# Performance work log

Measured on AMD Instinct MI355X. Metric: run time of the kernel, lower is better.

## Reference

```python
import jax, jax.numpy as jnp
import numpy as np

B, N, M, K, QK, GEO = 2, 16384, 4096, 16, 64, 18
EPS = 1e-5


def _conv1d(x, w, b):  # x [B,C,N], w [O,C] -> [B,O,N]  (1x1 Conv1d)
    return jnp.einsum('oc,bcn->bon', w, x) + b[None, :, None]


def _bn1d(x, g, bt):  # train-mode BatchNorm1d: batch stats over (B, N)
    m = x.mean(axis=(0, 2), keepdims=True)
    v = x.var(axis=(0, 2), keepdims=True)
    return (x - m) * jax.lax.rsqrt(v + EPS) * g[None, :, None] + bt[None, :, None]


def _conv2d(x, w, b):  # x [B,C,N,K], w [O,C] -> [B,O,N,K]  (1x1 Conv2d)
    return jnp.einsum('oc,bcnk->bonk', w, x) + b[None, :, None, None]


def _bn2d(x, g, bt):
    m = x.mean(axis=(0, 2, 3), keepdims=True)
    v = x.var(axis=(0, 2, 3), keepdims=True)
    return (x - m) * jax.lax.rsqrt(v + EPS) * g[None, :, None, None] + bt[None, :, None, None]


def _gather(t, idx):  # t [B,C,M], idx [B,N,K] -> [B,C,N,K]; t_g[b,c,n,j] = t[b,c,idx[b,n,j]]
    return jnp.take_along_axis(t[:, :, None, :], idx[:, None, :, :], axis=3)


def setup_inputs() -> dict:
    key = jax.random.key(0)
    ks = iter(jax.random.split(key, 40))
    def rn(shape, s=0.02):
        return jax.random.normal(next(ks), shape, jnp.float32) * s
    def z(c):
        return jnp.zeros((c,), jnp.float32)
    def o(c):
        return jnp.ones((c,), jnp.float32)
    return dict(
        xyz_hr=jax.random.normal(next(ks), (B, 3, N), jnp.float32),
        xyz_lr=jax.random.normal(next(ks), (B, 3, M), jnp.float32),
        val_lr=jax.random.normal(next(ks), (B, 6, M), jnp.float32),
        feat_hr=jax.random.normal(next(ks), (B, GEO, N), jnp.float32),
        feat_lr=jax.random.normal(next(ks), (B, GEO, M), jnp.float32),
        ge_w1=rn((QK, GEO)), ge_b1=z(QK), ge_g1=o(QK), ge_bt1=z(QK),
        ge_w2=rn((QK, QK)), ge_b2=z(QK), ge_g2=o(QK), ge_bt2=z(QK),
        sc_w=rn((QK, 6)), sc_b=z(QK), sh_w=rn((QK, 6)), sh_b=z(QK),
        q_w=rn((QK, QK)), q_b=z(QK), k_w=rn((QK, QK)), k_b=z(QK),
        bh_w1=rn((32, QK)), bh_b1=z(32), bh_g=o(32), bh_bt=z(32),
        bh_w2=rn((1, 32)), bh_b2=z(1),
        rp_w1=rn((QK, 3)), rp_b1=z(QK), rp_g=o(QK), rp_bt=z(QK),
        rp_w2=rn((QK, QK)), rp_b2=z(QK),
    )


def reference(xyz_hr, xyz_lr, val_lr, feat_hr, feat_lr,
              ge_w1, ge_b1, ge_g1, ge_bt1, ge_w2, ge_b2, ge_g2, ge_bt2,
              sc_w, sc_b, sh_w, sh_b, q_w, q_b, k_w, k_b,
              bh_w1, bh_b1, bh_g, bh_bt, bh_w2, bh_b2,
              rp_w1, rp_b1, rp_g, rp_bt, rp_w2, rp_b2):
    def geom_enc(x):
        x = jax.nn.relu(_bn1d(_conv1d(x, ge_w1, ge_b1), ge_g1, ge_bt1))
        return jax.nn.relu(_bn1d(_conv1d(x, ge_w2, ge_b2), ge_g2, ge_bt2))

    geom_hr = geom_enc(feat_hr)   # [B,QK,N]
    geom_lr = geom_enc(feat_lr)   # [B,QK,M]

    # val_lr has 6 channels -> FiLM modulation branch is taken
    scale = _conv1d(val_lr, sc_w, sc_b)
    shift = _conv1d(val_lr, sh_w, sh_b)
    geom_lr = geom_lr * (scale + 1.0) + shift

    bdy = jax.nn.relu(_bn1d(_conv1d(geom_hr, bh_w1, bh_b1), bh_g, bh_bt))
    bdy_prob = jax.nn.sigmoid(_conv1d(bdy, bh_w2, bh_b2))  # [B,1,N]

    Q = _conv1d(geom_hr, q_w, q_b)   # [B,QK,N]
    Kf = _conv1d(geom_lr, k_w, k_b)  # [B,QK,M]

    # kNN under no_grad: squared euclidean via expansion (same ordering as cdist)
    a = xyz_hr.transpose(0, 2, 1)  # [B,N,3]
    b = xyz_lr.transpose(0, 2, 1)  # [B,M,3]
    d2 = (jnp.sum(a * a, -1)[:, :, None] + jnp.sum(b * b, -1)[:, None, :]
          - 2.0 * jnp.einsum('bnc,bmc->bnm', a, b))
    d2 = jax.lax.stop_gradient(d2)
    _, idx = jax.lax.top_k(-d2, K)  # [B,N,K] indices of K nearest low-res points

    K_g = _gather(Kf, idx)            # [B,QK,N,K]
    xyz_lr_g = _gather(xyz_lr, idx)   # [B,3,N,K]
    rel_pos = xyz_hr[:, :, :, None] - xyz_lr_g
    pe = jax.nn.relu(_bn2d(_conv2d(rel_pos, rp_w1, rp_b1), rp_g, rp_bt))
    pos_enc = _conv2d(pe, rp_w2, rp_b2)  # [B,QK,N,K]

    scores = jnp.einsum('bcn,bcnk->bnk', Q, K_g + pos_enc) / jnp.sqrt(jnp.float32(QK))
    attn = jax.nn.softmax(scores, axis=-1)          # [B,N,K]
    val_g = _gather(val_lr, idx)                    # [B,6,N,K]
    out = jnp.einsum('bnk,bcnk->bcn', attn, val_g)  # [B,6,N]
    return out, bdy_prob
```

## Files before the change

kernel.cpp:

```cpp
#include <hip/hip_runtime.h>

#define BB 2
#define NN 16384
#define MM 4096
#define KK 16
#define CQ 64
#define GEOC 18
#define EPSV 1e-5
#define SPL 8

__device__ __forceinline__ float dist2f(float sa, float ax, float ay, float az, float4 p) {
#pragma clang fp contract(off)
  return (sa + p.w) - 2.0f * ((ax * p.x + ay * p.y) + az * p.z);
}

__device__ __forceinline__ void ce(float& a, float& b) {
  float lo = fminf(a, b), hi = fmaxf(a, b); a = lo; b = hi;
}
__device__ __forceinline__ void sort8(float* v) {
  ce(v[0],v[1]); ce(v[2],v[3]); ce(v[4],v[5]); ce(v[6],v[7]);
  ce(v[0],v[2]); ce(v[1],v[3]); ce(v[4],v[6]); ce(v[5],v[7]);
  ce(v[1],v[2]); ce(v[5],v[6]);
  ce(v[0],v[4]); ce(v[1],v[5]); ce(v[2],v[6]); ce(v[3],v[7]);
  ce(v[2],v[4]); ce(v[3],v[5]);
  ce(v[1],v[2]); ce(v[3],v[4]); ce(v[5],v[6]);
}
__device__ __forceinline__ void bitonic16(float* v) {
#pragma unroll
  for (int i = 0; i < 8; i++) ce(v[i], v[i + 8]);
  ce(v[0],v[4]); ce(v[1],v[5]); ce(v[2],v[6]); ce(v[3],v[7]);
  ce(v[8],v[12]); ce(v[9],v[13]); ce(v[10],v[14]); ce(v[11],v[15]);
  ce(v[0],v[2]); ce(v[1],v[3]); ce(v[4],v[6]); ce(v[5],v[7]);
  ce(v[8],v[10]); ce(v[9],v[11]); ce(v[12],v[14]); ce(v[13],v[15]);
  ce(v[0],v[1]); ce(v[2],v[3]); ce(v[4],v[5]); ce(v[6],v[7]);
  ce(v[8],v[9]); ce(v[10],v[11]); ce(v[12],v[13]); ce(v[14],v[15]);
}
__device__ __forceinline__ void merge16_8(float* dv, const float* t) {
  dv[8]  = fminf(dv[8],  t[7]);  dv[9]  = fminf(dv[9],  t[6]);
  dv[10] = fminf(dv[10], t[5]);  dv[11] = fminf(dv[11], t[4]);
  dv[12] = fminf(dv[12], t[3]);  dv[13] = fminf(dv[13], t[2]);
  dv[14] = fminf(dv[14], t[1]);  dv[15] = fminf(dv[15], t[0]);
  bitonic16(dv);
}

__global__ __launch_bounds__(256) void init_k(const float* __restrict__ xyz,
    const float* __restrict__ val, float* __restrict__ xyzT, float* __restrict__ valT,
    const float* __restrict__ qw, const float* __restrict__ qb, const float* __restrict__ w2,
    float* __restrict__ R, float* __restrict__ rb, int* __restrict__ hdr)
{
#pragma clang fp contract(off)
  if (blockIdx.x < 32) {
    int i = blockIdx.x * 256 + threadIdx.x;
    int b = i / MM, m = i % MM;
    float x = xyz[(b * 3 + 0) * MM + m];
    float y = xyz[(b * 3 + 1) * MM + m];
    float z = xyz[(b * 3 + 2) * MM + m];
    float sb = (x * x + y * y) + z * z;
    ((float4*)xyzT)[i] = make_float4(x, y, z, sb);
    float v0 = val[((size_t)b * 6 + 0) * MM + m];
    float v1 = val[((size_t)b * 6 + 1) * MM + m];
    float v2 = val[((size_t)b * 6 + 2) * MM + m];
    float v3 = val[((size_t)b * 6 + 3) * MM + m];
    float v4 = val[((size_t)b * 6 + 4) * MM + m];
    float v5 = val[((size_t)b * 6 + 5) * MM + m];
    ((float4*)valT)[2 * i]     = make_float4(v0, v1, v2, v3);
    ((float4*)valT)[2 * i + 1] = make_float4(v4, v5, 0.f, 0.f);
  } else {
    int t = threadIdx.x;
    for (int wd = t; wd < 1376; wd += 256) hdr[wd] = 0;
#pragma unroll
    for (int e = t * 16; e < t * 16 + 16; e++) {
      int o = e >> 6, i = e & 63;
      float acc = 0.f;
#pragma unroll
      for (int p = 0; p < CQ; p++) acc = fmaf(w2[p * CQ + o], qw[p * CQ + i], acc);
      R[e] = acc;
    }
    if (t < CQ) {
      float a = 0.f;
#pragma unroll
      for (int p = 0; p < CQ; p++) a = fmaf(w2[p * CQ + t], qb[p], a);
      rb[t] = a;
    }
  }
}

template<int CIN, int COUT, int OBLK, bool TOUT>
__device__ __forceinline__ void conv_body(int tid, const float* __restrict__ x,
    const float* __restrict__ W, const float* __restrict__ bias,
    const float* __restrict__ AB, float* __restrict__ y, int L)
{
  int g = tid / (BB * L);
  int i = tid % (BB * L);
  int b = i / L, n = i % L;
  const float* xp = x + (size_t)b * CIN * L + n;
  float xr[CIN];
#pragma unroll
  for (int c = 0; c < CIN; c++) {
    float v = xp[(size_t)c * L];
    if (AB) v = fmaxf(fmaf(v, AB[c], AB[CIN + c]), 0.f);
    xr[c] = v;
  }
#pragma unroll
  for (int oo = 0; oo < OBLK; oo++) {
    int o = g * OBLK + oo;
    float acc = bias ? bias[o] : 0.f;
#pragma unroll
    for (int c = 0; c < CIN; c++)
      acc = fmaf(W[(size_t)o * CIN + c], xr[c], acc);
    if (TOUT) y[((size_t)b * L + n) * COUT + o] = acc;
    else      y[((size_t)b * COUT + o) * L + n] = acc;
  }
}

template<int CIN, int COUT, int OBLK>
__global__ __launch_bounds__(256) void convhl_k(const float* __restrict__ xh,
    const float* __restrict__ xl, const float* __restrict__ W, const float* __restrict__ bias,
    const float* __restrict__ ABh, const float* __restrict__ ABl,
    float* __restrict__ yh, float* __restrict__ yl, int hb)
{
  if ((int)blockIdx.x < hb)
    conv_body<CIN, COUT, OBLK, false>(blockIdx.x * 256 + threadIdx.x, xh, W, bias, ABh, yh, NN);
  else
    conv_body<CIN, COUT, OBLK, false>((blockIdx.x - hb) * 256 + threadIdx.x, xl, W, bias, ABl, yl, MM);
}

template<int C, int NCH>
__device__ __forceinline__ void stats_body(int bid, const float* __restrict__ t, int L,
    const float* __restrict__ g, const float* __restrict__ bt,
    double* __restrict__ sums, int* __restrict__ counter, float* __restrict__ AB)
{
  int c = bid % C;
  int ch = bid / C;
  const size_t tot = (size_t)BB * L;
  const size_t slab = tot / NCH;
  size_t beg = slab * ch, end = beg + slab;
  double s = 0.0, ss = 0.0;
  for (size_t idx = beg + threadIdx.x; idx < end; idx += 256) {
    int b = (int)(idx / L); int i = (int)(idx % L);
    double v = t[((size_t)b * C + c) * L + i];
    s += v; ss += v * v;
  }
  for (int o = 32; o >= 1; o >>= 1) { s += __shfl_down(s, o); ss += __shfl_down(ss, o); }
  __shared__ double sh[8];
  __shared__ int lastf;
  int w = threadIdx.x >> 6;
  if ((threadIdx.x & 63) == 0) { sh[2 * w] = s; sh[2 * w + 1] = ss; }
  __syncthreads();
  if (threadIdx.x == 0) {
    for (int j = 1; j < 4; j++) { s += sh[2 * j]; ss += sh[2 * j + 1]; }
    atomicAdd(&sums[c], s);
    atomicAdd(&sums[C + c], ss);
    __threadfence();
    int old = atomicAdd(counter, 1);
    lastf = (old == C * NCH - 1) ? 1 : 0;
  }
  __syncthreads();
  if (lastf && threadIdx.x < C) {
    __threadfence();
    int cc = threadIdx.x;
    double S  = atomicAdd(&sums[cc], 0.0);
    double SS = atomicAdd(&sums[C + cc], 0.0);
    double nn = (double)BB * L;
    double mean = S / nn, var = SS / nn - mean * mean;
    double A = (double)g[cc] / sqrt(var + EPSV);
    AB[cc] = (float)A;
    AB[C + cc] = (float)((double)bt[cc] - mean * A);
  }
}

template<int C, int NCH>
__global__ __launch_bounds__(256) void statsone_k(const float* __restrict__ t, int L,
    const float* __restrict__ g, const float* __restrict__ bt,
    double* __restrict__ sums, int* __restrict__ counter, float* __restrict__ AB)
{
  stats_body<C, NCH>(blockIdx.x, t, L, g, bt, sums, counter, AB);
}

template<int C, int NCH>
__global__ __launch_bounds__(256) void statshl_k(const float* __restrict__ t0, int L0,
    const float* __restrict__ t1, int L1, const float* __restrict__ g,
    const float* __restrict__ bt, double* __restrict__ sums, int* __restrict__ ctrs,
    float* __restrict__ AB0, float* __restrict__ AB1)
{
  if ((int)blockIdx.x < C * NCH)
    stats_body<C, NCH>(blockIdx.x, t0, L0, g, bt, sums, ctrs, AB0);
  else
    stats_body<C, NCH>(blockIdx.x - C * NCH, t1, L1, g, bt, sums + 2 * C, ctrs + 1, AB1);
}

__global__ __launch_bounds__(256) void fk_k(const float* __restrict__ t2l,
    const float* __restrict__ ABl, const float* __restrict__ val,
    const float* __restrict__ scw, const float* __restrict__ scb,
    const float* __restrict__ shw, const float* __restrict__ shb,
    const float* __restrict__ kw, const float* __restrict__ kb,
    float* __restrict__ KfT)
{
  int tid = blockIdx.x * 256 + threadIdx.x;
  int g = tid & 7;
  int i = tid >> 3;
  int b = i / MM, m = i % MM;
  float v6[6];
#pragma unroll
  for (int j = 0; j < 6; j++) v6[j] = val[((size_t)b * 6 + j) * MM + m];
  float xr[CQ];
#pragma unroll
  for (int c = 0; c < CQ; c++) {
    float gv = fmaxf(fmaf(t2l[((size_t)b * CQ + c) * MM + m], ABl[c], ABl[CQ + c]), 0.f);
    float sc = scb[c], sh = shb[c];
#pragma unroll
    for (int j = 0; j < 6; j++) {
      sc = fmaf(scw[c * 6 + j], v6[j], sc);
      sh = fmaf(shw[c * 6 + j], v6[j], sh);
    }
    xr[c] = fmaf(gv, 1.f + sc, sh);
  }
#pragma unroll
  for (int oo = 0; oo < 8; oo++) {
    int o = g * 8 + oo;
    float acc = kb[o];
#pragma unroll
    for (int c = 0; c < CQ; c++) acc = fmaf(kw[o * CQ + c], xr[c], acc);
    KfT[(size_t)i * CQ + o] = acc;
  }
}

__global__ __launch_bounds__(256) void convbqq_k(const float* __restrict__ x,
    const float* __restrict__ bw, const float* __restrict__ bb,
    const float* __restrict__ Wq, const float* __restrict__ bq,
    const float* __restrict__ R, const float* __restrict__ rb,
    const float* __restrict__ AB, float* __restrict__ tb,
    float* __restrict__ Q, float* __restrict__ Qp)
{
  int tid = blockIdx.x * 256 + threadIdx.x;
  int g = tid / (BB * NN);
  int i = tid % (BB * NN);
  int b = i / NN, n = i % NN;
  const float* xp = x + (size_t)b * CQ * NN + n;
  float xr[CQ];
#pragma unroll
  for (int c = 0; c < CQ; c++)
    xr[c] = fmaxf(fmaf(xp[(size_t)c * NN], AB[c], AB[CQ + c]), 0.f);
  const float* W; const float* bias; float* y; int o0;
  if (g < 2)      { W = bw; bias = bb; y = tb; o0 = g * 16;       }
  else if (g < 6) { W = Wq; bias = bq; y = Q;  o0 = (g - 2) * 16; }
  else            { W = R;  bias = rb; y = Qp; o0 = (g - 6) * 16; }
  int COUTL = (g < 2) ? 32 : CQ;
#pragma unroll
  for (int oo = 0; oo < 16; oo++) {
    int o = o0 + oo;
    float acc = bias[o];
#pragma unroll
    for (int c = 0; c < CQ; c++) acc = fmaf(W[o * CQ + c], xr[c], acc);
    y[((size_t)b * COUTL + o) * NN + n] = acc;
  }
}

__global__ __launch_bounds__(256) void knnA_k(const float* __restrict__ xyz_hr,
    const float* __restrict__ xyzT, float* __restrict__ theta)
{
#pragma clang fp contract(off)
  int tid = blockIdx.x * 256 + threadIdx.x;
  int s = tid & (SPL - 1);
  int qi = tid / SPL;
  int b = qi / NN, n = qi % NN;
  float ax = xyz_hr[(b * 3 + 0) * NN + n];
  float ay = xyz_hr[(b * 3 + 1) * NN + n];
  float az = xyz_hr[(b * 3 + 2) * NN + n];
  float sa = (ax * ax + ay * ay) + az * az;
  const float4* __restrict__ Ps = ((const float4*)xyzT) + (size_t)b * MM + s;
  float dv[16];
#pragma unroll
  for (int j = 0; j < 16; j++) dv[j] = 3.4e38f;
  for (int j = 0; j < MM / SPL; j += 8) {
    float t[8];
#pragma unroll
    for (int u = 0; u < 8; u++) {
      float4 p = Ps[(size_t)(j + u) * SPL];
      t[u] = dist2f(sa, ax, ay, az, p);
    }
    sort8(t);
    merge16_8(dv, t);
  }
#pragma unroll
  for (int mask = 1; mask <= 4; mask <<= 1) {
    float c[16];
#pragma unroll
    for (int j = 0; j < 16; j++) c[j] = __shfl_xor(dv[15 - j], mask);
#pragma unroll
    for (int j = 0; j < 16; j++) dv[j] = fminf(dv[j], c[j]);
    bitonic16(dv);
  }
  if (s == 0) theta[qi] = dv[15];
}

__global__ __launch_bounds__(256) void knnC_k(const float* __restrict__ xyz_hr,
    const float* __restrict__ xyzT, const float* __restrict__ theta,
    int* __restrict__ idx_out, double* __restrict__ mompart)
{
#pragma clang fp contract(off)
  __shared__ int s_clt[32], s_ceq[32];
  __shared__ int s_lt[32][16];
  __shared__ int s_eq[32][64];
  __shared__ int s_sel[32][16];
  __shared__ float s_mom[4][9];
  int w = threadIdx.x >> 6, l = threadIdx.x & 63;
  int qblk = blockIdx.x * 32;
  int b = qblk / NN;
  int n0 = qblk % NN + w * 8;
  if (threadIdx.x < 32) { s_clt[threadIdx.x] = 0; s_ceq[threadIdx.x] = 0; }
  __syncthreads();
  float qx[8], qy[8], qz[8], qs[8], th[8];
#pragma unroll
  for (int q = 0; q < 8; q++) {
    qx[q] = xyz_hr[(b * 3 + 0) * NN + n0 + q];
    qy[q] = xyz_hr[(b * 3 + 1) * NN + n0 + q];
    qz[q] = xyz_hr[(b * 3 + 2) * NN + n0 + q];
    qs[q] = (qx[q] * qx[q] + qy[q] * qy[q]) + qz[q] * qz[q];
    th[q] = theta[(size_t)b * NN + n0 + q];
  }
  const float4* __restrict__ P = ((const float4*)xyzT) + (size_t)b * MM;
  for (int j = 0; j < MM / 64; j++) {
    int m = j * 64 + l;
    float4 p = P[m];
#pragma unroll
    for (int q = 0; q < 8; q++) {
      float d = (qs[q] + p.w) - 2.0f * ((qx[q] * p.x + qy[q] * p.y) + qz[q] * p.z);
      int qq = w * 8 + q;
      if (d < th[q]) {
        int pos = atomicAdd(&s_clt[qq], 1);
        if (pos < 16) s_lt[qq][pos] = m;
      } else if (d == th[q]) {
        int pos = atomicAdd(&s_ceq[qq], 1);
        if (pos < 64) s_eq[qq][pos] = m;
      }
    }
  }
  __syncthreads();
  if (threadIdx.x < 32) {
    int qq = threadIdx.x;
    int clt = s_clt[qq]; if (clt > 16) clt = 16;
    int ceq = s_ceq[qq]; if (ceq > 64) ceq = 64;
    for (int j = 0; j < clt; j++) s_sel[qq][j] = s_lt[qq][j];
    int need = KK - clt;
    for (int t = 0; t < need; t++) {
      int best = 0x7fffffff, bp = 0;
      for (int j = 0; j < ceq; j++) { int v = s_eq[qq][j]; if (v < best) { best = v; bp = j; } }
      s_sel[qq][clt + t] = best;
      s_eq[qq][bp] = 0x7fffffff;
    }
    size_t base = ((size_t)qblk + qq) * KK;
    for (int j = 0; j < KK; j++) idx_out[base + j] = s_sel[qq][j];
  }
  __syncthreads();
  float t9[9];
#pragma unroll
  for (int j = 0; j < 9; j++) t9[j] = 0.f;
  for (int slot = threadIdx.x; slot < 512; slot += 256) {
    int qq = slot >> 4, jj = slot & 15;
    int nn_ = qblk % NN + qq;
    float ax = xyz_hr[(b * 3 + 0) * NN + nn_];
    float ay = xyz_hr[(b * 3 + 1) * NN + nn_];
    float az = xyz_hr[(b * 3 + 2) * NN + nn_];
    float4 p = P[s_sel[qq][jj]];
    float rx = ax - p.x, ry = ay - p.y, rz = az - p.z;
    t9[0] += rx; t9[1] += ry; t9[2] += rz;
    t9[3] += rx * rx; t9[4] += ry * ry; t9[5] += rz * rz;
    t9[6] += rx * ry; t9[7] += rx * rz; t9[8] += ry * rz;
  }
#pragma unroll
  for (int j = 0; j < 9; j++)
    for (int o = 32; o >= 1; o >>= 1) t9[j] += __shfl_down(t9[j], o);
  if (l == 0) { for (int j = 0; j < 9; j++) s_mom[w][j] = t9[j]; }
  __syncthreads();
  if (threadIdx.x == 0) {
    double* op = mompart + (size_t)blockIdx.x * 9;
    for (int j = 0; j < 9; j++)
      op[j] = (double)s_mom[0][j] + (double)s_mom[1][j] + (double)s_mom[2][j] + (double)s_mom[3][j];
  }
}

__global__ __launch_bounds__(256) void mom2_k(const double* __restrict__ part, int nblk,
    const float* __restrict__ w1, const float* __restrict__ b1,
    const float* __restrict__ g, const float* __restrict__ bt, float* __restrict__ AB)
{
  double acc[9];
#pragma unroll
  for (int j = 0; j < 9; j++) acc[j] = 0.0;
  for (int blk = threadIdx.x; blk < nblk; blk += 256) {
    const double* p = part + (size_t)blk * 9;
#pragma unroll
    for (int j = 0; j < 9; j++) acc[j] += p[j];
  }
#pragma unroll
  for (int j = 0; j < 9; j++)
    for (int o = 32; o >= 1; o >>= 1) acc[j] += __shfl_down(acc[j], o);
  __shared__ double sh[4][9];
  __shared__ double mo[9];
  int w = threadIdx.x >> 6, l = threadIdx.x & 63;
  if (l == 0) { for (int j = 0; j < 9; j++) sh[w][j] = acc[j]; }
  __syncthreads();
  if (threadIdx.x == 0) {
    for (int wv = 1; wv < 4; wv++) for (int j = 0; j < 9; j++) sh[0][j] += sh[wv][j];
    for (int j = 0; j < 9; j++) mo[j] = sh[0][j];
  }
  __syncthreads();
  if (threadIdx.x < CQ) {
    int c = threadIdx.x;
    double cnt = (double)BB * NN * KK;
    double mx = mo[0]/cnt, my = mo[1]/cnt, mz = mo[2]/cnt;
    double cxx = mo[3]/cnt - mx*mx, cyy = mo[4]/cnt - my*my, czz = mo[5]/cnt - mz*mz;
    double cxy = mo[6]/cnt - mx*my, cxz = mo[7]/cnt - mx*mz, cyz = mo[8]/cnt - my*mz;
    double wx = w1[c*3], wy = w1[c*3+1], wz = w1[c*3+2];
    double mean = wx*mx + wy*my + wz*mz + (double)b1[c];
    double var = wx*wx*cxx + wy*wy*cyy + wz*wz*czz + 2.0*(wx*wy*cxy + wx*wz*cxz + wy*wz*cyz);
    double A = (double)g[c] / sqrt(var + EPSV);
    AB[c] = (float)A;
    AB[CQ + c] = (float)((double)bt[c] - mean * A);
  }
}

__global__ __launch_bounds__(256) void attn_k(
    const float* __restrict__ Q, const float* __restrict__ Qp,
    const float* __restrict__ KfT, const int* __restrict__ idxb,
    const float* __restrict__ xyzT, const float* __restrict__ valT,
    const float* __restrict__ xyz_hr, const float* __restrict__ AB,
    const float* __restrict__ w1, const float* __restrict__ b1,
    const float* __restrict__ b2, float* __restrict__ out,
    const float* __restrict__ tb, const float* __restrict__ ABb,
    const float* __restrict__ bhw2, const float* __restrict__ bhb2)
{
  __shared__ float q_s[CQ * 16], qp_s[CQ * 16];
  if (blockIdx.x >= 2048) {
    int i = (blockIdx.x - 2048) * 256 + threadIdx.x;
    int b = i / NN, n = i % NN;
    float acc = bhb2[0];
#pragma unroll
    for (int c = 0; c < 32; c++) {
      float v = tb[((size_t)b * 32 + c) * NN + n];
      v = fmaxf(fmaf(v, ABb[c], ABb[32 + c]), 0.f);
      acc = fmaf(bhw2[c], v, acc);
    }
    out[(size_t)BB * 6 * NN + i] = 1.f / (1.f + expf(-acc));
    return;
  }
  const int ngrp = NN / 16;
  int b = blockIdx.x / ngrp;
  int n0 = (blockIdx.x % ngrp) * 16;
  for (int t = threadIdx.x; t < CQ * 16; t += 256) {
    int c = t >> 4, j = t & 15;
    q_s[t]  = Q [((size_t)b * CQ + c) * NN + n0 + j];
    qp_s[t] = Qp[((size_t)b * CQ + c) * NN + n0 + j];
  }
  __syncthreads();
  int q = threadIdx.x >> 4, k = threadIdx.x & 15;
  int n = n0 + q;
  int id = idxb[((size_t)b * NN + n) * KK + k];
  float ax = xyz_hr[(b * 3 + 0) * NN + n];
  float ay = xyz_hr[(b * 3 + 1) * NN + n];
  float az = xyz_hr[(b * 3 + 2) * NN + n];
  float4 pl = ((const float4*)xyzT)[(size_t)b * MM + id];
  float rx = ax - pl.x, ry = ay - pl.y, rz = az - pl.z;
  const float4* kg = (const float4*)(KfT + ((size_t)b * MM + id) * CQ);
  float s = 0.f;
#pragma unroll
  for (int c4 = 0; c4 < CQ / 4; c4++) {
    float4 g4 = kg[c4];
    float ga[4] = {g4.x, g4.y, g4.z, g4.w};
#pragma unroll
    for (int u = 0; u < 4; u++) {
      int c = 4 * c4 + u;
      float t0 = fmaf(w1[c * 3 + 0], rx, fmaf(w1[c * 3 + 1], ry, w1[c * 3 + 2] * rz)) + b1[c];
      float pe = fmaxf(fmaf(t0, AB[c], AB[CQ + c]), 0.f);
      s = fmaf(q_s[c * 16 + q], ga[u] + b2[c], s);
      s = fmaf(qp_s[c * 16 + q], pe, s);
    }
  }
  s *= 0.125f;
  float mx = s;
#pragma unroll
  for (int o = 8; o >= 1; o >>= 1) mx = fmaxf(mx, __shfl_xor(mx, o, 16));
  float p = expf(s - mx);
  float sum = p;
#pragma unroll
  for (int o = 8; o >= 1; o >>= 1) sum += __shfl_xor(sum, o, 16);
  float attn = p / sum;
  const float4* vt = (const float4*)(valT + ((size_t)b * MM + id) * 8);
  float4 va = vt[0], vb = vt[1];
  float oc[6] = {attn*va.x, attn*va.y, attn*va.z, attn*va.w, attn*vb.x, attn*vb.y};
#pragma unroll
  for (int c = 0; c < 6; c++) {
    float a = oc[c];
#pragma unroll
    for (int o = 8; o >= 1; o >>= 1) a += __shfl_xor(a, o, 16);
    oc[c] = a;
  }
  if (k == 0) {
#pragma unroll
    for (int c = 0; c < 6; c++) out[((size_t)b * 6 + c) * NN + n] = oc[c];
  }
}

extern "C" void kernel_launch(void* const* d_in, const int* in_sizes, int n_in,
                              void* d_out, int out_size, void* d_ws, size_t ws_size,
                              hipStream_t stream)
{
  const float* xyz_hr = (const float*)d_in[0];
  const float* xyz_lr = (const float*)d_in[1];
  const float* val_lr = (const float*)d_in[2];
  const float* feat_hr= (const float*)d_in[3];
  const float* feat_lr= (const float*)d_in[4];
  const float* ge_w1 = (const float*)d_in[5];
  const float* ge_b1 = (const float*)d_in[6];
  const float* ge_g1 = (const float*)d_in[7];
  const float* ge_bt1= (const float*)d_in[8];
  const float* ge_w2 = (const float*)d_in[9];
  const float* ge_b2 = (const float*)d_in[10];
  const float* ge_g2 = (const float*)d_in[11];
  const float* ge_bt2= (const float*)d_in[12];
  const float* sc_w = (const float*)d_in[13];
  const float* sc_b = (const float*)d_in[14];
  const float* sh_w = (const float*)d_in[15];
  const float* sh_b = (const float*)d_in[16];
  const float* q_w  = (const float*)d_in[17];
  const float* q_b  = (const float*)d_in[18];
  const float* k_w  = (const float*)d_in[19];
  const float* k_b  = (const float*)d_in[20];
  const float* bh_w1= (const float*)d_in[21];
  const float* bh_b1= (const float*)d_in[22];
  const float* bh_g = (const float*)d_in[23];
  const float* bh_bt= (const float*)d_in[24];
  const float* bh_w2= (const float*)d_in[25];
  const float* bh_b2= (const float*)d_in[26];
  const float* rp_w1= (const float*)d_in[27];
  const float* rp_b1= (const float*)d_in[28];
  const float* rp_g = (const float*)d_in[29];
  const float* rp_bt= (const float*)d_in[30];
  const float* rp_w2= (const float*)d_in[31];
  const float* rp_b2= (const float*)d_in[32];
  float* out = (float*)d_out;

  int*    hdr  = (int*)d_ws;
  int*    ctrs = (int*)((char*)d_ws + 96);
  double* sums = (double*)((char*)d_ws + 128);
  float*  base = (float*)((char*)d_ws + 5504);
  float* AB1h = base;
  float* AB2h = base + 128;
  float* AB1l = base + 256;
  float* AB2l = base + 384;
  float* ABb  = base + 512;
  float* AB2d = base + 576;
  float* big  = base + 768;
  float* t1_hr = big;
  float* t2_hr = t1_hr + 2097152;
  float* Qb    = t2_hr + 2097152;
  float* Qp    = Qb    + 2097152;
  float* t1_lr = Qp    + 2097152;
  float* t2_lr = t1_lr + 524288;
  float* Rbuf  = t2_lr + 524288;
  float* KfT   = Rbuf  + 524288;
  float* tb    = KfT   + 524288;
  float* xyzT  = tb    + 1048576;
  float* valT  = xyzT  + 32768;
  int*   idxb  = (int*)(valT + 65536);
  float* theta = Qb;
  double* mompart = (double*)Qp;
  float* Rw    = Rbuf;
  float* rbv   = Rbuf + 4096;

  init_k<<<33, 256, 0, stream>>>(xyz_lr, val_lr, xyzT, valT, q_w, q_b, rp_w2, Rw, rbv, hdr);

  knnA_k<<<(BB * NN * SPL) / 256, 256, 0, stream>>>(xyz_hr, xyzT, theta);
  knnC_k<<<(BB * NN) / 32, 256, 0, stream>>>(xyz_hr, xyzT, theta, idxb, mompart);
  mom2_k<<<1, 256, 0, stream>>>(mompart, (BB * NN) / 32, rp_w1, rp_b1, rp_g, rp_bt, AB2d);

  convhl_k<GEOC, CQ, 16><<<640, 256, 0, stream>>>(feat_hr, feat_lr, ge_w1, ge_b1,
                                                  nullptr, nullptr, t1_hr, t1_lr, 512);
  statshl_k<CQ, 8><<<1024, 256, 0, stream>>>(t1_hr, NN, t1_lr, MM, ge_g1, ge_bt1,
                                             sums, ctrs + 0, AB1h, AB1l);
  convhl_k<CQ, CQ, 16><<<640, 256, 0, stream>>>(t1_hr, t1_lr, ge_w2, ge_b2,
                                                AB1h, AB1l, t2_hr, t2_lr, 512);
  statshl_k<CQ, 8><<<1024, 256, 0, stream>>>(t2_hr, NN, t2_lr, MM, ge_g2, ge_bt2,
                                             sums + 256, ctrs + 2, AB2h, AB2l);

  fk_k<<<256, 256, 0, stream>>>(t2_lr, AB2l, val_lr, sc_w, sc_b, sh_w, sh_b,
                                k_w, k_b, KfT);

  convbqq_k<<<1280, 256, 0, stream>>>(t2_hr, bh_w1, bh_b1, q_w, q_b, Rw, rbv,
                                      AB2h, tb, Qb, Qp);
  statsone_k<32, 8><<<256, 256, 0, stream>>>(tb, NN, bh_g, bh_bt, sums + 512, ctrs + 4, ABb);

  attn_k<<<2048 + 128, 256, 0, stream>>>(Qb, Qp, KfT, idxb, xyzT, valT, xyz_hr, AB2d,
                                         rp_w1, rp_b1, rp_b2, out, tb, ABb, bh_w2, bh_b2);
}
```

Measured before the change: 530.9 us.

## Fuse kNN, conv and BatchNorm stats kernels into fewer combined launches

Merges the separate 1x1 conv and BatchNorm-statistics kernels by computing per-channel sums in shared memory right after each conv block, using a last-block-done counter to finalize the scale and shift. The independent kNN passes are co-scheduled in the same launches as the conv layers, and mom2, fk and convbqq are grouped into one kernel. This cuts the launch count from about ten to four and removes the re-reads of the conv outputs for statistics. In exchange it adds shared-memory reductions and atomics, gives heterogeneous blocks in each grid, and moves mompart to its own buffer.

New measurement: 463.4 us. 1.15x faster.

```diff
diff --git a/kernel.cpp b/kernel.cpp
--- a/kernel.cpp
+++ b/kernel.cpp
@@ -85,182 +85,10 @@
   }
 }
 
-template<int CIN, int COUT, int OBLK, bool TOUT>
-__device__ __forceinline__ void conv_body(int tid, const float* __restrict__ x,
-    const float* __restrict__ W, const float* __restrict__ bias,
-    const float* __restrict__ AB, float* __restrict__ y, int L)
-{
-  int g = tid / (BB * L);
-  int i = tid % (BB * L);
-  int b = i / L, n = i % L;
-  const float* xp = x + (size_t)b * CIN * L + n;
-  float xr[CIN];
-#pragma unroll
-  for (int c = 0; c < CIN; c++) {
-    float v = xp[(size_t)c * L];
-    if (AB) v = fmaxf(fmaf(v, AB[c], AB[CIN + c]), 0.f);
-    xr[c] = v;
-  }
-#pragma unroll
-  for (int oo = 0; oo < OBLK; oo++) {
-    int o = g * OBLK + oo;
-    float acc = bias ? bias[o] : 0.f;
-#pragma unroll
-    for (int c = 0; c < CIN; c++)
-      acc = fmaf(W[(size_t)o * CIN + c], xr[c], acc);
-    if (TOUT) y[((size_t)b * L + n) * COUT + o] = acc;
-    else      y[((size_t)b * COUT + o) * L + n] = acc;
-  }
-}
-
-template<int CIN, int COUT, int OBLK>
-__global__ __launch_bounds__(256) void convhl_k(const float* __restrict__ xh,
-    const float* __restrict__ xl, const float* __restrict__ W, const float* __restrict__ bias,
-    const float* __restrict__ ABh, const float* __restrict__ ABl,
-    float* __restrict__ yh, float* __restrict__ yl, int hb)
-{
-  if ((int)blockIdx.x < hb)
-    conv_body<CIN, COUT, OBLK, false>(blockIdx.x * 256 + threadIdx.x, xh, W, bias, ABh, yh, NN);
-  else
-    conv_body<CIN, COUT, OBLK, false>((blockIdx.x - hb) * 256 + threadIdx.x, xl, W, bias, ABl, yl, MM);
-}
-
-template<int C, int NCH>
-__device__ __forceinline__ void stats_body(int bid, const float* __restrict__ t, int L,
-    const float* __restrict__ g, const float* __restrict__ bt,
-    double* __restrict__ sums, int* __restrict__ counter, float* __restrict__ AB)
-{
-  int c = bid % C;
-  int ch = bid / C;
-  const size_t tot = (size_t)BB * L;
-  const size_t slab = tot / NCH;
-  size_t beg = slab * ch, end = beg + slab;
-  double s = 0.0, ss = 0.0;
-  for (size_t idx = beg + threadIdx.x; idx < end; idx += 256) {
-    int b = (int)(idx / L); int i = (int)(idx % L);
-    double v = t[((size_t)b * C + c) * L + i];
-    s += v; ss += v * v;
-  }
-  for (int o = 32; o >= 1; o >>= 1) { s += __shfl_down(s, o); ss += __shfl_down(ss, o); }
-  __shared__ double sh[8];
-  __shared__ int lastf;
-  int w = threadIdx.x >> 6;
-  if ((threadIdx.x & 63) == 0) { sh[2 * w] = s; sh[2 * w + 1] = ss; }
-  __syncthreads();
-  if (threadIdx.x == 0) {
-    for (int j = 1; j < 4; j++) { s += sh[2 * j]; ss += sh[2 * j + 1]; }
-    atomicAdd(&sums[c], s);
-    atomicAdd(&sums[C + c], ss);
-    __threadfence();
-    int old = atomicAdd(counter, 1);
-    lastf = (old == C * NCH - 1) ? 1 : 0;
-  }
-  __syncthreads();
-  if (lastf && threadIdx.x < C) {
-    __threadfence();
-    int cc = threadIdx.x;
-    double S  = atomicAdd(&sums[cc], 0.0);
-    double SS = atomicAdd(&sums[C + cc], 0.0);
-    double nn = (double)BB * L;
-    double mean = S / nn, var = SS / nn - mean * mean;
-    double A = (double)g[cc] / sqrt(var + EPSV);
-    AB[cc] = (float)A;
-    AB[C + cc] = (float)((double)bt[cc] - mean * A);
-  }
-}
-
-template<int C, int NCH>
-__global__ __launch_bounds__(256) void statsone_k(const float* __restrict__ t, int L,
-    const float* __restrict__ g, const float* __restrict__ bt,
-    double* __restrict__ sums, int* __restrict__ counter, float* __restrict__ AB)
-{
-  stats_body<C, NCH>(blockIdx.x, t, L, g, bt, sums, counter, AB);
-}
-
-template<int C, int NCH>
-__global__ __launch_bounds__(256) void statshl_k(const float* __restrict__ t0, int L0,
-    const float* __restrict__ t1, int L1, const float* __restrict__ g,
-    const float* __restrict__ bt, double* __restrict__ sums, int* __restrict__ ctrs,
-    float* __restrict__ AB0, float* __restrict__ AB1)
-{
-  if ((int)blockIdx.x < C * NCH)
-    stats_body<C, NCH>(blockIdx.x, t0, L0, g, bt, sums, ctrs, AB0);
-  else
-    stats_body<C, NCH>(blockIdx.x - C * NCH, t1, L1, g, bt, sums + 2 * C, ctrs + 1, AB1);
-}
-
-__global__ __launch_bounds__(256) void fk_k(const float* __restrict__ t2l,
-    const float* __restrict__ ABl, const float* __restrict__ val,
-    const float* __restrict__ scw, const float* __restrict__ scb,
-    const float* __restrict__ shw, const float* __restrict__ shb,
-    const float* __restrict__ kw, const float* __restrict__ kb,
-    float* __restrict__ KfT)
-{
-  int tid = blockIdx.x * 256 + threadIdx.x;
-  int g = tid & 7;
-  int i = tid >> 3;
-  int b = i / MM, m = i % MM;
-  float v6[6];
-#pragma unroll
-  for (int j = 0; j < 6; j++) v6[j] = val[((size_t)b * 6 + j) * MM + m];
-  float xr[CQ];
-#pragma unroll
-  for (int c = 0; c < CQ; c++) {
-    float gv = fmaxf(fmaf(t2l[((size_t)b * CQ + c) * MM + m], ABl[c], ABl[CQ + c]), 0.f);
-    float sc = scb[c], sh = shb[c];
-#pragma unroll
-    for (int j = 0; j < 6; j++) {
-      sc = fmaf(scw[c * 6 + j], v6[j], sc);
-      sh = fmaf(shw[c * 6 + j], v6[j], sh);
-    }
-    xr[c] = fmaf(gv, 1.f + sc, sh);
-  }
-#pragma unroll
-  for (int oo = 0; oo < 8; oo++) {
-    int o = g * 8 + oo;
-    float acc = kb[o];
-#pragma unroll
-    for (int c = 0; c < CQ; c++) acc = fmaf(kw[o * CQ + c], xr[c], acc);
-    KfT[(size_t)i * CQ + o] = acc;
-  }
-}
-
-__global__ __launch_bounds__(256) void convbqq_k(const float* __restrict__ x,
-    const float* __restrict__ bw, const float* __restrict__ bb,
-    const float* __restrict__ Wq, const float* __restrict__ bq,
-    const float* __restrict__ R, const float* __restrict__ rb,
-    const float* __restrict__ AB, float* __restrict__ tb,
-    float* __restrict__ Q, float* __restrict__ Qp)
-{
-  int tid = blockIdx.x * 256 + threadIdx.x;
-  int g = tid / (BB * NN);
-  int i = tid % (BB * NN);
-  int b = i / NN, n = i % NN;
-  const float* xp = x + (size_t)b * CQ * NN + n;
-  float xr[CQ];
-#pragma unroll
-  for (int c = 0; c < CQ; c++)
-    xr[c] = fmaxf(fmaf(xp[(size_t)c * NN], AB[c], AB[CQ + c]), 0.f);
-  const float* W; const float* bias; float* y; int o0;
-  if (g < 2)      { W = bw; bias = bb; y = tb; o0 = g * 16;       }
-  else if (g < 6) { W = Wq; bias = bq; y = Q;  o0 = (g - 2) * 16; }
-  else            { W = R;  bias = rb; y = Qp; o0 = (g - 6) * 16; }
-  int COUTL = (g < 2) ? 32 : CQ;
-#pragma unroll
-  for (int oo = 0; oo < 16; oo++) {
-    int o = o0 + oo;
-    float acc = bias[o];
-#pragma unroll
-    for (int c = 0; c < CQ; c++) acc = fmaf(W[o * CQ + c], xr[c], acc);
-    y[((size_t)b * COUTL + o) * NN + n] = acc;
-  }
-}
-
-__global__ __launch_bounds__(256) void knnA_k(const float* __restrict__ xyz_hr,
+__device__ __forceinline__ void knnA_body(int tid, const float* __restrict__ xyz_hr,
     const float* __restrict__ xyzT, float* __restrict__ theta)
 {
 #pragma clang fp contract(off)
-  int tid = blockIdx.x * 256 + threadIdx.x;
   int s = tid & (SPL - 1);
   int qi = tid / SPL;
   int b = qi / NN, n = qi % NN;
@@ -294,18 +122,121 @@
   if (s == 0) theta[qi] = dv[15];
 }
 
-__global__ __launch_bounds__(256) void knnC_k(const float* __restrict__ xyz_hr,
+template<int CIN>
+__device__ __forceinline__ void convstats_hl(int cbid,
+    const float* __restrict__ xh, const float* __restrict__ xl,
+    const float* __restrict__ W, const float* __restrict__ bias,
+    const float* __restrict__ ABh_in, const float* __restrict__ ABl_in,
+    float* __restrict__ yh, float* __restrict__ yl,
+    double* __restrict__ sums, int* __restrict__ ctr,
+    const float* __restrict__ gw, const float* __restrict__ btw,
+    float* __restrict__ ABh_out, float* __restrict__ ABl_out,
+    float* red, int* plastf)
+{
+  bool ish = cbid < 512;
+  const float* x = ish ? xh : xl;
+  const float* ABi = ish ? ABh_in : ABl_in;
+  float* y = ish ? yh : yl;
+  int L = ish ? NN : MM;
+  int lb = ish ? cbid : cbid - 512;
+  int tid = lb * 256 + threadIdx.x;
+  int g = tid / (BB * L);
+  int i = tid % (BB * L);
+  int b = i / L, n = i % L;
+  const float* xp = x + (size_t)b * CIN * L + n;
+  float xr[CIN];
+#pragma unroll
+  for (int c = 0; c < CIN; c++) {
+    float v = xp[(size_t)c * L];
+    if (ABi) v = fmaxf(fmaf(v, ABi[c], ABi[CIN + c]), 0.f);
+    xr[c] = v;
+  }
+  float acc[16];
+#pragma unroll
+  for (int oo = 0; oo < 16; oo++) {
+    int o = g * 16 + oo;
+    float a = bias[o];
+#pragma unroll
+    for (int c = 0; c < CIN; c++) a = fmaf(W[(size_t)o * CIN + c], xr[c], a);
+    acc[oo] = a;
+    y[((size_t)b * CQ + o) * L + n] = a;
+  }
+#pragma unroll
+  for (int oo = 0; oo < 16; oo++) red[oo * 257 + threadIdx.x] = acc[oo];
+  __syncthreads();
+  float* r2 = red + 16 * 257;
+  int t = threadIdx.x;
+  if (t < 128) {
+    int oo = t >> 3, seg = t & 7;
+    float s = 0.f, ss = 0.f;
+    for (int j = seg * 32; j < seg * 32 + 32; j++) {
+      float v = red[oo * 257 + j]; s += v; ss += v * v;
+    }
+    r2[(oo * 8 + seg) * 2] = s; r2[(oo * 8 + seg) * 2 + 1] = ss;
+  }
+  __syncthreads();
+  if (t < 16) {
+    double s = 0.0, ss = 0.0;
+    for (int j = 0; j < 8; j++) { s += r2[(t * 8 + j) * 2]; ss += r2[(t * 8 + j) * 2 + 1]; }
+    int c = g * 16 + t;
+    int base = ish ? 0 : 128;
+    atomicAdd(&sums[base + c], s);
+    atomicAdd(&sums[base + 64 + c], ss);
+  }
+  __syncthreads();
+  if (t == 0) {
+    __threadfence();
+    int old = atomicAdd(ctr, 1);
+    *plastf = (old == 640 - 1) ? 1 : 0;
+  }
+  __syncthreads();
+  if (*plastf && t < 128) {
+    bool fh = t < 64;
+    int c = fh ? t : t - 64;
+    int base = fh ? 0 : 128;
+    double S  = atomicAdd(&sums[base + c], 0.0);
+    double SS = atomicAdd(&sums[base + 64 + c], 0.0);
+    double nn2 = (double)BB * (fh ? NN : MM);
+    double mean = S / nn2, var = SS / nn2 - mean * mean;
+    double A = (double)gw[c] / sqrt(var + EPSV);
+    float* ABo = fh ? ABh_out : ABl_out;
+    ABo[c] = (float)A;
+    ABo[64 + c] = (float)((double)btw[c] - mean * A);
+  }
+}
+
+__global__ __launch_bounds__(256) void k2_k(const float* __restrict__ xyz_hr,
+    const float* __restrict__ xyzT, float* __restrict__ theta,
+    const float* __restrict__ feat_hr, const float* __restrict__ feat_lr,
+    const float* __restrict__ w1, const float* __restrict__ b1,
+    double* __restrict__ sums, int* __restrict__ ctr,
+    const float* __restrict__ gw, const float* __restrict__ btw,
+    float* __restrict__ t1h, float* __restrict__ t1l,
+    float* __restrict__ AB1h, float* __restrict__ AB1l)
+{
+  __shared__ __align__(16) float smem[16 * 257 + 256];
+  __shared__ int lastf;
+  if (blockIdx.x < 1024) {
+    knnA_body(blockIdx.x * 256 + threadIdx.x, xyz_hr, xyzT, theta);
+  } else {
+    convstats_hl<GEOC>(blockIdx.x - 1024, feat_hr, feat_lr, w1, b1, nullptr, nullptr,
+                       t1h, t1l, sums, ctr, gw, btw, AB1h, AB1l, smem, &lastf);
+  }
+}
+
+__device__ __forceinline__ void knnC_body(int cbid, const float* __restrict__ xyz_hr,
     const float* __restrict__ xyzT, const float* __restrict__ theta,
-    int* __restrict__ idx_out, double* __restrict__ mompart)
+    int* __restrict__ idx_out, double* __restrict__ mompart, float* smemf)
 {
 #pragma clang fp contract(off)
-  __shared__ int s_clt[32], s_ceq[32];
-  __shared__ int s_lt[32][16];
-  __shared__ int s_eq[32][64];
-  __shared__ int s_sel[32][16];
-  __shared__ float s_mom[4][9];
+  int* s_clt = (int*)smemf;
+  int* s_ceq = s_clt + 32;
+  int* s_lt  = s_ceq + 32;
+  int* s_eq  = s_lt + 512;
+  int* s_sel = s_eq + 2048;
+  float* s_mom = (float*)(s_sel + 512);
   int w = threadIdx.x >> 6, l = threadIdx.x & 63;
-  int qblk = blockIdx.x * 32;
+  int qblk = cbid * 32;
   int b = qblk / NN;
   int n0 = qblk % NN + w * 8;
   if (threadIdx.x < 32) { s_clt[threadIdx.x] = 0; s_ceq[threadIdx.x] = 0; }
@@ -329,10 +260,10 @@
       int qq = w * 8 + q;
       if (d < th[q]) {
         int pos = atomicAdd(&s_clt[qq], 1);
-        if (pos < 16) s_lt[qq][pos] = m;
+        if (pos < 16) s_lt[qq * 16 + pos] = m;
       } else if (d == th[q]) {
         int pos = atomicAdd(&s_ceq[qq], 1);
-        if (pos < 64) s_eq[qq][pos] = m;
+        if (pos < 64) s_eq[qq * 64 + pos] = m;
       }
     }
   }
@@ -341,16 +272,16 @@
     int qq = threadIdx.x;
     int clt = s_clt[qq]; if (clt > 16) clt = 16;
     int ceq = s_ceq[qq]; if (ceq > 64) ceq = 64;
-    for (int j = 0; j < clt; j++) s_sel[qq][j] = s_lt[qq][j];
+    for (int j = 0; j < clt; j++) s_sel[qq * 16 + j] = s_lt[qq * 16 + j];
     int need = KK - clt;
     for (int t = 0; t < need; t++) {
       int best = 0x7fffffff, bp = 0;
-      for (int j = 0; j < ceq; j++) { int v = s_eq[qq][j]; if (v < best) { best = v; bp = j; } }
-      s_sel[qq][clt + t] = best;
-      s_eq[qq][bp] = 0x7fffffff;
+      for (int j = 0; j < ceq; j++) { int v = s_eq[qq * 64 + j]; if (v < best) { best = v; bp = j; } }
+      s_sel[qq * 16 + clt + t] = best;
+      s_eq[qq * 64 + bp] = 0x7fffffff;
     }
     size_t base = ((size_t)qblk + qq) * KK;
-    for (int j = 0; j < KK; j++) idx_out[base + j] = s_sel[qq][j];
+    for (int j = 0; j < KK; j++) idx_out[base + j] = s_sel[qq * 16 + j];
   }
   __syncthreads();
   float t9[9];
@@ -362,7 +293,7 @@
     float ax = xyz_hr[(b * 3 + 0) * NN + nn_];
     float ay = xyz_hr[(b * 3 + 1) * NN + nn_];
     float az = xyz_hr[(b * 3 + 2) * NN + nn_];
-    float4 p = P[s_sel[qq][jj]];
+    float4 p = P[s_sel[qq * 16 + jj]];
     float rx = ax - p.x, ry = ay - p.y, rz = az - p.z;
     t9[0] += rx; t9[1] += ry; t9[2] += rz;
     t9[3] += rx * rx; t9[4] += ry * ry; t9[5] += rz * rz;
@@ -371,19 +302,43 @@
 #pragma unroll
   for (int j = 0; j < 9; j++)
     for (int o = 32; o >= 1; o >>= 1) t9[j] += __shfl_down(t9[j], o);
-  if (l == 0) { for (int j = 0; j < 9; j++) s_mom[w][j] = t9[j]; }
+  if (l == 0) { for (int j = 0; j < 9; j++) s_mom[w * 9 + j] = t9[j]; }
   __syncthreads();
   if (threadIdx.x == 0) {
-    double* op = mompart + (size_t)blockIdx.x * 9;
+    double* op = mompart + (size_t)cbid * 9;
     for (int j = 0; j < 9; j++)
-      op[j] = (double)s_mom[0][j] + (double)s_mom[1][j] + (double)s_mom[2][j] + (double)s_mom[3][j];
-  }
-}
-
-__global__ __launch_bounds__(256) void mom2_k(const double* __restrict__ part, int nblk,
+      op[j] = (double)s_mom[j] + (double)s_mom[9 + j] + (double)s_mom[18 + j] + (double)s_mom[27 + j];
+  }
+}
+
+__global__ __launch_bounds__(256) void k3_k(const float* __restrict__ xyz_hr,
+    const float* __restrict__ xyzT, const float* __restrict__ theta,
+    int* __restrict__ idxb, double* __restrict__ mompart,
+    const float* __restrict__ t1h, const float* __restrict__ t1l,
+    const float* __restrict__ w2, const float* __restrict__ b2,
+    const float* __restrict__ AB1h, const float* __restrict__ AB1l,
+    double* __restrict__ sums, int* __restrict__ ctr,
+    const float* __restrict__ gw, const float* __restrict__ btw,
+    float* __restrict__ t2h, float* __restrict__ t2l,
+    float* __restrict__ AB2h, float* __restrict__ AB2l)
+{
+  __shared__ __align__(16) float smem[16 * 257 + 256];
+  __shared__ int lastf;
+  if (blockIdx.x < 1024) {
+    knnC_body(blockIdx.x, xyz_hr, xyzT, theta, idxb, mompart, smem);
+  } else {
+    convstats_hl<CQ>(blockIdx.x - 1024, t1h, t1l, w2, b2, AB1h, AB1l,
+                     t2h, t2l, sums, ctr, gw, btw, AB2h, AB2l, smem, &lastf);
+  }
+}
+
+__device__ __forceinline__ void mom2_body(const double* __restrict__ part, int nblk,
     const float* __restrict__ w1, const float* __restrict__ b1,
-    const float* __restrict__ g, const float* __restrict__ bt, float* __restrict__ AB)
-{
+    const float* __restrict__ g, const float* __restrict__ bt, float* __restrict__ AB,
+    float* smemf)
+{
+  double* sh = (double*)smemf;
+  double* mo = sh + 36;
   double acc[9];
 #pragma unroll
   for (int j = 0; j < 9; j++) acc[j] = 0.0;
@@ -395,14 +350,11 @@
 #pragma unroll
   for (int j = 0; j < 9; j++)
     for (int o = 32; o >= 1; o >>= 1) acc[j] += __shfl_down(acc[j], o);
-  __shared__ double sh[4][9];
-  __shared__ double mo[9];
   int w = threadIdx.x >> 6, l = threadIdx.x & 63;
-  if (l == 0) { for (int j = 0; j < 9; j++) sh[w][j] = acc[j]; }
+  if (l == 0) { for (int j = 0; j < 9; j++) sh[w * 9 + j] = acc[j]; }
   __syncthreads();
   if (threadIdx.x == 0) {
-    for (int wv = 1; wv < 4; wv++) for (int j = 0; j < 9; j++) sh[0][j] += sh[wv][j];
-    for (int j = 0; j < 9; j++) mo[j] = sh[0][j];
+    for (int j = 0; j < 9; j++) mo[j] = sh[j] + sh[9 + j] + sh[18 + j] + sh[27 + j];
   }
   __syncthreads();
   if (threadIdx.x < CQ) {
@@ -417,6 +369,144 @@
     double A = (double)g[c] / sqrt(var + EPSV);
     AB[c] = (float)A;
     AB[CQ + c] = (float)((double)bt[c] - mean * A);
+  }
+}
+
+__device__ __forceinline__ void fk_body(int fb, const float* __restrict__ t2l,
+    const float* __restrict__ ABl, const float* __restrict__ val,
+    const float* __restrict__ scw, const float* __restrict__ scb,
+    const float* __restrict__ shw, const float* __restrict__ shb,
+    const float* __restrict__ kw, const float* __restrict__ kb,
+    float* __restrict__ KfT)
+{
+  int tid = fb * 256 + threadIdx.x;
+  int g = tid & 3;
+  int i = tid >> 2;
+  int b = i / MM, m = i % MM;
+  float v6[6];
+#pragma unroll
+  for (int j = 0; j < 6; j++) v6[j] = val[((size_t)b * 6 + j) * MM + m];
+  float xr[CQ];
+#pragma unroll
+  for (int c = 0; c < CQ; c++) {
+    float gv = fmaxf(fmaf(t2l[((size_t)b * CQ + c) * MM + m], ABl[c], ABl[CQ + c]), 0.f);
+    float sc = scb[c], sh = shb[c];
+#pragma unroll
+    for (int j = 0; j < 6; j++) {
+      sc = fmaf(scw[c * 6 + j], v6[j], sc);
+      sh = fmaf(shw[c * 6 + j], v6[j], sh);
+    }
+    xr[c] = fmaf(gv, 1.f + sc, sh);
+  }
+#pragma unroll
+  for (int oo = 0; oo < 16; oo++) {
+    int o = g * 16 + oo;
+    float acc = kb[o];
+#pragma unroll
+    for (int c = 0; c < CQ; c++) acc = fmaf(kw[o * CQ + c], xr[c], acc);
+    KfT[(size_t)i * CQ + o] = acc;
+  }
+}
+
+__device__ __forceinline__ void convbqq_body(int cb, const float* __restrict__ x,
+    const float* __restrict__ bw, const float* __restrict__ bb,
+    const float* __restrict__ Wq, const float* __restrict__ bq,
+    const float* __restrict__ R, const float* __restrict__ rb,
+    const float* __restrict__ AB, float* __restrict__ tb,
+    float* __restrict__ Q, float* __restrict__ Qp,
+    double* __restrict__ sums, int* __restrict__ ctr,
+    const float* __restrict__ gw, const float* __restrict__ btw,
+    float* __restrict__ ABb, float* red, int* plastf)
+{
+  int tid = cb * 256 + threadIdx.x;
+  int g = tid / (BB * NN);
+  int i = tid % (BB * NN);
+  int b = i / NN, n = i % NN;
+  const float* xp = x + (size_t)b * CQ * NN + n;
+  float xr[CQ];
+#pragma unroll
+  for (int c = 0; c < CQ; c++)
+    xr[c] = fmaxf(fmaf(xp[(size_t)c * NN], AB[c], AB[CQ + c]), 0.f);
+  const float* W; const float* bias; float* y; int o0; int COUTL;
+  if (g < 2)      { W = bw; bias = bb; y = tb; o0 = g * 16;       COUTL = 32; }
+  else if (g < 6) { W = Wq; bias = bq; y = Q;  o0 = (g - 2) * 16; COUTL = CQ; }
+  else            { W = R;  bias = rb; y = Qp; o0 = (g - 6) * 16; COUTL = CQ; }
+  float acc[16];
+#pragma unroll
+  for (int oo = 0; oo < 16; oo++) {
+    int o = o0 + oo;
+    float a = bias[o];
+#pragma unroll
+    for (int c = 0; c < CQ; c++) a = fmaf(W[o * CQ + c], xr[c], a);
+    acc[oo] = a;
+    y[((size_t)b * COUTL + o) * NN + n] = a;
+  }
+  if (g >= 2) return;
+#pragma unroll
+  for (int oo = 0; oo < 16; oo++) red[oo * 257 + threadIdx.x] = acc[oo];
+  __syncthreads();
+  float* r2 = red + 16 * 257;
+  int t = threadIdx.x;
+  if (t < 128) {
+    int oo = t >> 3, seg = t & 7;
+    float s = 0.f, ss = 0.f;
+    for (int j = seg * 32; j < seg * 32 + 32; j++) {
+      float v = red[oo * 257 + j]; s += v; ss += v * v;
+    }
+    r2[(oo * 8 + seg) * 2] = s; r2[(oo * 8 + seg) * 2 + 1] = ss;
+  }
+  __syncthreads();
+  if (t < 16) {
+    double s = 0.0, ss = 0.0;
+    for (int j = 0; j < 8; j++) { s += r2[(t * 8 + j) * 2]; ss += r2[(t * 8 + j) * 2 + 1]; }
+    int c = g * 16 + t;
+    atomicAdd(&sums[c], s);
+    atomicAdd(&sums[32 + c], ss);
+  }
+  __syncthreads();
+  if (t == 0) {
+    __threadfence();
+    int old = atomicAdd(ctr, 1);
+    *plastf = (old == 256 - 1) ? 1 : 0;
+  }
+  __syncthreads();
+  if (*plastf && t < 32) {
+    int c = t;
+    double S  = atomicAdd(&sums[c], 0.0);
+    double SS = atomicAdd(&sums[32 + c], 0.0);
+    double nn2 = (double)BB * NN;
+    double mean = S / nn2, var = SS / nn2 - mean * mean;
+    double A = (double)gw[c] / sqrt(var + EPSV);
+    ABb[c] = (float)A;
+    ABb[32 + c] = (float)((double)btw[c] - mean * A);
+  }
+}
+
+__global__ __launch_bounds__(256) void k4_k(
+    const double* __restrict__ mompart,
+    const float* __restrict__ rp_w1, const float* __restrict__ rp_b1,
+    const float* __restrict__ rp_g, const float* __restrict__ rp_bt, float* __restrict__ AB2d,
+    const float* __restrict__ t2l, const float* __restrict__ AB2l, const float* __restrict__ val,
+    const float* __restrict__ scw, const float* __restrict__ scb,
+    const float* __restrict__ shw, const float* __restrict__ shb,
+    const float* __restrict__ kw, const float* __restrict__ kb, float* __restrict__ KfT,
+    const float* __restrict__ t2h, const float* __restrict__ bw, const float* __restrict__ bb,
+    const float* __restrict__ Wq, const float* __restrict__ bq,
+    const float* __restrict__ R, const float* __restrict__ rb,
+    const float* __restrict__ AB2h, float* __restrict__ tb,
+    float* __restrict__ Q, float* __restrict__ Qp,
+    double* __restrict__ sums3, int* __restrict__ ctr3,
+    const float* __restrict__ bh_g, const float* __restrict__ bh_bt, float* __restrict__ ABb)
+{
+  __shared__ __align__(16) float smem[16 * 257 + 256];
+  __shared__ int lastf;
+  if (blockIdx.x == 0) {
+    mom2_body(mompart, 1024, rp_w1, rp_b1, rp_g, rp_bt, AB2d, smem);
+  } else if (blockIdx.x <= 128) {
+    fk_body(blockIdx.x - 1, t2l, AB2l, val, scw, scb, shw, shb, kw, kb, KfT);
+  } else {
+    convbqq_body(blockIdx.x - 129, t2h, bw, bb, Wq, bq, R, rb, AB2h, tb, Q, Qp,
+                 sums3, ctr3, bh_g, bh_bt, ABb, smem, &lastf);
   }
 }
 
@@ -563,32 +653,24 @@
   float* xyzT  = tb    + 1048576;
   float* valT  = xyzT  + 32768;
   int*   idxb  = (int*)(valT + 65536);
+  double* mompart = (double*)(idxb + BB * NN * KK);
   float* theta = Qb;
-  double* mompart = (double*)Qp;
   float* Rw    = Rbuf;
   float* rbv   = Rbuf + 4096;
 
   init_k<<<33, 256, 0, stream>>>(xyz_lr, val_lr, xyzT, valT, q_w, q_b, rp_w2, Rw, rbv, hdr);
 
-  knnA_k<<<(BB * NN * SPL) / 256, 256, 0, stream>>>(xyz_hr, xyzT, theta);
-  knnC_k<<<(BB * NN) / 32, 256, 0, stream>>>(xyz_hr, xyzT, theta, idxb, mompart);
-  mom2_k<<<1, 256, 0, stream>>>(mompart, (BB * NN) / 32, rp_w1, rp_b1, rp_g, rp_bt, AB2d);
-
-  convhl_k<GEOC, CQ, 16><<<640, 256, 0, stream>>>(feat_hr, feat_lr, ge_w1, ge_b1,
-                                                  nullptr, nullptr, t1_hr, t1_lr, 512);
-  statshl_k<CQ, 8><<<1024, 256, 0, stream>>>(t1_hr, NN, t1_lr, MM, ge_g1, ge_bt1,
-                                             sums, ctrs + 0, AB1h, AB1l);
-  convhl_k<CQ, CQ, 16><<<640, 256, 0, stream>>>(t1_hr, t1_lr, ge_w2, ge_b2,
-                                                AB1h, AB1l, t2_hr, t2_lr, 512);
-  statshl_k<CQ, 8><<<1024, 256, 0, stream>>>(t2_hr, NN, t2_lr, MM, ge_g2, ge_bt2,
-                                             sums + 256, ctrs + 2, AB2h, AB2l);
-
-  fk_k<<<256, 256, 0, stream>>>(t2_lr, AB2l, val_lr, sc_w, sc_b, sh_w, sh_b,
-                                k_w, k_b, KfT);
-
-  convbqq_k<<<1280, 256, 0, stream>>>(t2_hr, bh_w1, bh_b1, q_w, q_b, Rw, rbv,
-                                      AB2h, tb, Qb, Qp);
-  statsone_k<32, 8><<<256, 256, 0, stream>>>(tb, NN, bh_g, bh_bt, sums + 512, ctrs + 4, ABb);
+  k2_k<<<1664, 256, 0, stream>>>(xyz_hr, xyzT, theta, feat_hr, feat_lr, ge_w1, ge_b1,
+                                 sums, ctrs + 0, ge_g1, ge_bt1, t1_hr, t1_lr, AB1h, AB1l);
+
+  k3_k<<<1664, 256, 0, stream>>>(xyz_hr, xyzT, theta, idxb, mompart, t1_hr, t1_lr,
+                                 ge_w2, ge_b2, AB1h, AB1l, sums + 256, ctrs + 1,
+                                 ge_g2, ge_bt2, t2_hr, t2_lr, AB2h, AB2l);
+
+  k4_k<<<1409, 256, 0, stream>>>(mompart, rp_w1, rp_b1, rp_g, rp_bt, AB2d,
+                                 t2_lr, AB2l, val_lr, sc_w, sc_b, sh_w, sh_b, k_w, k_b, KfT,
+                                 t2_hr, bh_w1, bh_b1, q_w, q_b, Rw, rbv, AB2h, tb, Qb, Qp,
+                                 sums + 512, ctrs + 2, bh_g, bh_bt, ABb);
 
   attn_k<<<2048 + 128, 256, 0, stream>>>(Qb, Qp, KfT, idxb, xyzT, valT, xyz_hr, AB2d,
                                          rp_w1, rp_b1, rp_b2, out, tb, ABb, bh_w2, bh_b2);
```
